# Performance work log

Hardware: AMD Instinct MI355X
Metric: run time of the kernel (lower is better)

The kernel has to match this reference:

```python
import jax, jax.numpy as jnp
import numpy as np

B, S, L, H, E, V = 32, 48, 48, 1024, 1024, 32000


def setup_inputs() -> dict:
    key = jax.random.key(0)
    ks = jax.random.split(key, 16)
    s = 0.02
    return {
        "label": jax.random.randint(ks[0], (B, S), 0, V),
        "init_hidden": jax.random.normal(ks[1], (1, B, H), jnp.float32),
        "encoder_output": jax.random.normal(ks[2], (B, L, H), jnp.float32),
        "emb": jax.random.normal(ks[3], (V, E), jnp.float32) * s,
        "attn_W": jax.random.normal(ks[4], (2 * H, L), jnp.float32) * s,
        "attn_b": jnp.zeros((L,), jnp.float32),
        "comb_W": jax.random.normal(ks[5], (2 * H, H), jnp.float32) * s,
        "comb_b": jnp.zeros((H,), jnp.float32),
        "W_ih": jax.random.normal(ks[6], (E, 3 * H), jnp.float32) * s,
        "W_hh": jax.random.normal(ks[7], (H, 3 * H), jnp.float32) * s,
        "b_ih": jnp.zeros((3 * H,), jnp.float32),
        "b_hh": jnp.zeros((3 * H,), jnp.float32),
        "out_W": jax.random.normal(ks[8], (H, V), jnp.float32) * s,
        "out_b": jnp.zeros((V,), jnp.float32),
    }


def _decode(label, init_hidden, encoder_output, emb, attn_W, attn_b,
            comb_W, comb_b, W_ih, W_hh, b_ih, b_hh, out_W, out_b):
    # Teacher forcing (teaching_force_rate=1.0): inputs are relu(embedding(label[:, i]))
    xs = jax.nn.relu(emb[label])            # (B, S, E)
    xs = jnp.transpose(xs, (1, 0, 2))       # (S, B, E) for scan

    def step(h, xe):                        # h: (B,H), xe: (B,E)
        # Attention: Linear(cat(emb, hidden)) -> nn.Softmax() on a 3D (B,1,L)
        # tensor, which in torch defaults to dim=0 (the batch dim) -- replicated.
        sim = jnp.concatenate([xe, h], axis=-1) @ attn_W + attn_b   # (B, L)
        w = jax.nn.softmax(sim, axis=0)                             # over batch (faithful)
        ctx = jnp.einsum('bl,blh->bh', w, encoder_output)           # bmm
        g = jax.nn.relu(jnp.concatenate([ctx, xe], axis=-1) @ comb_W + comb_b)  # (B,H)
        # Single GRU step (torch gate order: r, z, n)
        gx = g @ W_ih + b_ih
        gh = h @ W_hh + b_hh
        xr, xz, xn = jnp.split(gx, 3, axis=-1)
        hr, hz, hn = jnp.split(gh, 3, axis=-1)
        r = jax.nn.sigmoid(xr + hr)
        z = jax.nn.sigmoid(xz + hz)
        n = jnp.tanh(xn + r * hn)
        h_new = (1.0 - z) * n + z * h
        out = jax.nn.log_softmax(h_new @ out_W + out_b, axis=-1)    # (B, V)
        return h_new, out

    _, outs = jax.lax.scan(step, init_hidden[0], xs)   # outs: (S, B, V)
    return jnp.transpose(outs, (1, 0, 2))              # (B, S, V)


def reference(label, init_hidden, encoder_output, emb, attn_W, attn_b,
              comb_W, comb_b, W_ih, W_hh, b_ih, b_hh, out_W, out_b):
    return _decode(label, init_hidden, encoder_output, emb, attn_W, attn_b,
                   comb_W, comb_b, W_ih, W_hh, b_ih, b_hh, out_W, out_b)
```

## Files before the change

kernel.cpp:

```cpp
#include <hip/hip_runtime.h>

#define NB 32
#define NS 48
#define NL 48
#define NH 1024
#define NE 1024
#define NV 32000
#define NR (NS*NB)
#define K3H 3072
#define RA_BLOCKS 64
#define RB_BLOCKS 128
#define RC_BLOCKS 64
#define NBLK_FULL (RA_BLOCKS + RB_BLOCKS + RC_BLOCKS)

typedef unsigned short u16;
typedef __bf16 bf16x8 __attribute__((ext_vector_type(8)));
typedef unsigned short ushort8 __attribute__((ext_vector_type(8)));
typedef float f32x4 __attribute__((ext_vector_type(4)));
typedef unsigned int uint4v __attribute__((ext_vector_type(4)));

__device__ __forceinline__ float bf2f(u16 x) {
    union { unsigned u; float f; } c; c.u = ((unsigned)x) << 16; return c.f;
}
__device__ __forceinline__ u16 f2bf(float f) {
    union { float f; unsigned u; } c; c.f = f;
    unsigned r = (c.u + 0x7FFFu + ((c.u >> 16) & 1u)) >> 16;
    return (u16)r;
}
__device__ __forceinline__ f32x4 mfma16(bf16x8 a, bf16x8 b, f32x4 c) {
    return __builtin_amdgcn_mfma_f32_16x16x32_bf16(a, b, c, 0, 0, 0);
}
__device__ __forceinline__ void gld_lds16(const void* g, void* l) {
    __builtin_amdgcn_global_load_lds((const __attribute__((address_space(1))) void*)g,
                                     (__attribute__((address_space(3))) void*)l, 16, 0, 0);
}

__device__ __forceinline__ void st16_coh(void* p, uint4v v) {
    asm volatile("global_store_dwordx4 %0, %1, off sc0 sc1" :: "v"(p), "v"(v) : "memory");
}
__device__ __forceinline__ void waitb(const int* line, int tgt) {
    if (tgt <= 0) return;
    int guard = 0; int v;
    for (;;) {
        asm volatile("global_load_dword %0, %1, off sc0 sc1\n\ts_waitcnt vmcnt(0)"
                     : "=v"(v) : "v"(line) : "memory");
        if (v >= tgt) return;
        __builtin_amdgcn_s_sleep(1);
        if (++guard > (1 << 20)) return;
    }
}
__device__ __forceinline__ void arrive2(int* cnt, int* superc, int* bcast, int lineMask, int val) {
    asm volatile("s_waitcnt vmcnt(0)" ::: "memory");
    int prev = __hip_atomic_fetch_add(cnt, 1, __ATOMIC_RELAXED, __HIP_MEMORY_SCOPE_AGENT);
    if ((prev & lineMask) == lineMask) {
        int p2 = __hip_atomic_fetch_add(superc, 1, __ATOMIC_RELAXED, __HIP_MEMORY_SCOPE_AGENT);
        if ((p2 & 7) == 7) {
#pragma unroll
            for (int i = 0; i < 24; ++i)
                asm volatile("global_store_dword %0, %1, off sc0 sc1"
                             :: "v"(bcast + i * 64), "v"(val) : "memory");
        }
    }
}

__global__ __launch_bounds__(256) void transpose_cast(const float* __restrict__ src, int K, int N,
                                                      char* __restrict__ dst, int bf16out) {
    __shared__ float tile[32][33];
    int k0 = blockIdx.y * 32, n0 = blockIdx.x * 32;
    int tx = threadIdx.x & 31, ty = threadIdx.x >> 5;
    for (int i = 0; i < 4; ++i) {
        int n = n0 + tx;
        float v = (n < N) ? src[(size_t)(k0 + ty + i*8) * N + n] : 0.f;
        tile[ty + i*8][tx] = v;
    }
    __syncthreads();
    for (int i = 0; i < 4; ++i) {
        int n = n0 + ty + i*8;
        int k = k0 + tx;
        if (n < N) {
            float v = tile[tx][ty + i*8];
            if (bf16out) ((u16*)dst)[(size_t)n * K + k] = f2bf(v);
            else         ((float*)dst)[(size_t)n * K + k] = v;
        }
    }
}

__global__ __launch_bounds__(256) void prep_inputs(const int* __restrict__ label, const float* __restrict__ emb,
                                                   const float* __restrict__ enc, const float* __restrict__ inith,
                                                   u16* __restrict__ xe, u16* __restrict__ encb, u16* __restrict__ hallx) {
    int blk = blockIdx.x, t = threadIdx.x;
    if (blk < NR) {
        int s = blk >> 5, b = blk & 31;
        int lab = label[b * NS + s];
        const float* src = emb + (size_t)lab * NE;
        u16* dst = xe + (size_t)blk * NE;
        for (int i = t; i < NE; i += 256) { float v = src[i]; dst[i] = f2bf(v > 0.f ? v : 0.f); }
    } else if (blk < 2 * NR) {
        int r = blk - NR;
        const float* src = enc + (size_t)r * NH;
        u16* dst = encb + (size_t)r * NH;
        for (int i = t; i < NH; i += 256) dst[i] = f2bf(src[i]);
    } else {
        int b = blk - 2 * NR;
        const float* src = inith + (size_t)b * NH;
        u16* dst = hallx + (size_t)b * NH;
        for (int i = t; i < NH; i += 256) dst[i] = f2bf(src[i]);
    }
}

__global__ __launch_bounds__(384) void simxe2_kernel(const u16* __restrict__ xe, const u16* __restrict__ aw1t,
                                                     const float* __restrict__ attnB, float* __restrict__ simxe) {
    int r = blockIdx.x, t = threadIdx.x;
    int l = t >> 3, part = t & 7;
    const u16* x = xe + (size_t)r * 1024 + part * 128;
    const u16* ww = aw1t + (size_t)l * 1024 + part * 128;
    float acc = 0.f;
#pragma unroll
    for (int k = 0; k < 128; k += 8) {
        ushort8 xv = *reinterpret_cast<const ushort8*>(x + k);
        ushort8 wv = *reinterpret_cast<const ushort8*>(ww + k);
#pragma unroll
        for (int u = 0; u < 8; ++u) acc += bf2f(xv[u]) * bf2f(wv[u]);
    }
    acc += __shfl_xor(acc, 1);
    acc += __shfl_xor(acc, 2);
    acc += __shfl_xor(acc, 4);
    if (part == 0) simxe[(size_t)r * NL + l] = acc + attnB[l];
}

template<int MODE>
__global__ __launch_bounds__(256) void gemm_bf16(const u16* __restrict__ A, const u16* __restrict__ Bt,
                                                 void* __restrict__ Cout, const float* __restrict__ bias, int N) {
    __shared__ u16 ldsA[128 * 64];
    __shared__ u16 ldsB[128 * 64];
    const int t = threadIdx.x;
    const int lane = t & 63, w = t >> 6;
    const int wm = w >> 1, wn = w & 1;
    const int m0 = blockIdx.x * 128, n0 = blockIdx.y * 128;
    f32x4 acc[4][4] = {};
    for (int kt = 0; kt < 16; ++kt) {
        const int k0 = kt * 64;
#pragma unroll
        for (int i = 0; i < 4; ++i) {
            int chunk = i * 256 + t;
            int row = chunk >> 3, slot = chunk & 7;
            int srck = ((slot ^ (row & 7)) * 8);
            const u16* ga = A  + (size_t)(m0 + row) * 1024 + k0 + srck;
            const u16* gb = Bt + (size_t)(n0 + row) * 1024 + k0 + srck;
            u16* la = ldsA + (size_t)(i * 256 + w * 64) * 8;
            u16* lb = ldsB + (size_t)(i * 256 + w * 64) * 8;
            gld_lds16(ga, la);
            gld_lds16(gb, lb);
        }
        asm volatile("s_waitcnt vmcnt(0)" ::: "memory");
        __syncthreads();
#pragma unroll
        for (int kk = 0; kk < 2; ++kk) {
            bf16x8 a[4], b[4];
#pragma unroll
            for (int f = 0; f < 4; ++f) {
                int rowA = wm * 64 + f * 16 + (lane & 15);
                int slotA = (kk * 4 + (lane >> 4)) ^ (rowA & 7);
                a[f] = *reinterpret_cast<const bf16x8*>(ldsA + rowA * 64 + slotA * 8);
                int rowB = wn * 64 + f * 16 + (lane & 15);
                int slotB = (kk * 4 + (lane >> 4)) ^ (rowB & 7);
                b[f] = *reinterpret_cast<const bf16x8*>(ldsB + rowB * 64 + slotB * 8);
            }
#pragma unroll
            for (int fm = 0; fm < 4; ++fm)
#pragma unroll
                for (int fn = 0; fn < 4; ++fn)
                    acc[fm][fn] = mfma16(a[fm], b[fn], acc[fm][fn]);
        }
        __syncthreads();
    }
#pragma unroll
    for (int fm = 0; fm < 4; ++fm) {
#pragma unroll
        for (int fn = 0; fn < 4; ++fn) {
#pragma unroll
            for (int rr = 0; rr < 4; ++rr) {
                int m = m0 + wm * 64 + fm * 16 + (lane >> 4) * 4 + rr;
                int n = n0 + wn * 64 + fn * 16 + (lane & 15);
                float v = acc[fm][fn][rr];
                if (bias) v += bias[n];
                if (MODE == 0)      ((float*)Cout)[(size_t)m * N + n] = v;
                else if (MODE == 2) ((u16*)Cout)[(size_t)m * N + n] = f2bf(v);
                else if (MODE == 1)
                    ((float*)Cout)[((size_t)(m & 31) * NS + (m >> 5)) * NV + n] = v;
                else
                    ((u16*)Cout)[((size_t)(m & 31) * NS + (m >> 5)) * NV + n] = f2bf(v);
            }
        }
    }
}

__global__ __launch_bounds__(512) void recurrence8(
    const float* __restrict__ simxe, const u16* __restrict__ gxe,
    const u16* __restrict__ P, const u16* __restrict__ aw2t,
    const u16* __restrict__ whht, const u16* __restrict__ wiht,
    const float* __restrict__ b_ih, const float* __restrict__ b_hh,
    u16* __restrict__ g_rot, u16* __restrict__ hallx,
    const float* __restrict__ outW, const float* __restrict__ outB,
    u16* __restrict__ outWT, u16* __restrict__ logit, int* __restrict__ bar)
{
    __shared__ __align__(16) char smem[155776];
    int* cntA   = bar;
    int* cntB   = bar + 512;
    int* superA = bar + 1024;
    int* superB = bar + 1088;
    int* bcastA = bar + 1152;
    int* bcastB = bar + 2688;
    int* cntC   = bar + 4224;
    const int blk = blockIdx.x, t = threadIdx.x;
    const int lane = t & 63, w = t >> 6;
    const int r16 = lane & 15, kg = lane >> 4;

    if (blk < RA_BLOCKS) {
        int* myB = bcastB + (blk % 24) * 64;
        const int b = blk >> 1, half = blk & 1;
        u16*   W2T  = (u16*)smem;
        u16*   Pl   = (u16*)(smem + 99072);
        float* siml = (float*)(smem + 148224);
        float* wl   = (float*)(smem + 154496);
        u16*   gtmp = (u16*)(smem + 154752);
        for (int idx = t; idx < 48 * 1024; idx += 512) {
            int l = idx >> 10, k = idx & 1023;
            W2T[l * 1032 + k] = aw2t[idx];
        }
        for (int idx = t; idx < 48 * 512; idx += 512) {
            int l = idx >> 9, j = idx & 511;
            Pl[idx] = P[((size_t)(b * 48 + l)) * NH + half * 512 + j];
        }
        __syncthreads();
        const int mt = w & 1, nt = w >> 1;
        const int m0 = mt * 16, n0 = nt * 16;

        for (int s = 0; s < NS; ++s) {
            float gxev = bf2f(gxe[((size_t)(s * 32 + b)) * NH + half * 512 + t]);
            float sxv0 = 0.f, sxv1 = 0.f, sxv2 = 0.f, sxv3 = 0.f;
            if (w < 6) {
                const float* sxe = simxe + (size_t)(s * 32) * NL;
                sxv0 = sxe[(m0 + kg * 4 + 0) * NL + n0 + r16];
                sxv1 = sxe[(m0 + kg * 4 + 1) * NL + n0 + r16];
                sxv2 = sxe[(m0 + kg * 4 + 2) * NL + n0 + r16];
                sxv3 = sxe[(m0 + kg * 4 + 3) * NL + n0 + r16];
            }
            if (t == 0) waitb(myB, s);
            __syncthreads();
            const u16* hprev = hallx + (size_t)s * (NB * NH);
            if (w < 6) {
                f32x4 acc0; f32x4 acc1 = {};
                acc0[0] = sxv0; acc0[1] = sxv1; acc0[2] = sxv2; acc0[3] = sxv3;
                const u16* aP = hprev + (size_t)(m0 + r16) * NH + kg * 8;
                const u16* bP = W2T + (n0 + r16) * 1032 + kg * 8;
#pragma unroll
                for (int k = 0; k < 1024; k += 64) {
                    acc0 = mfma16(*reinterpret_cast<const bf16x8*>(aP + k),
                                  *reinterpret_cast<const bf16x8*>(bP + k), acc0);
                    acc1 = mfma16(*reinterpret_cast<const bf16x8*>(aP + k + 32),
                                  *reinterpret_cast<const bf16x8*>(bP + k + 32), acc1);
                }
#pragma unroll
                for (int rr = 0; rr < 4; ++rr)
                    siml[(m0 + kg * 4 + rr) * 49 + n0 + r16] = acc0[rr] + acc1[rr];
            }
            __syncthreads();
            if (t < 384) {
                int l = t >> 3, p = t & 7;
                float v0 = siml[(p * 4 + 0) * 49 + l];
                float v1 = siml[(p * 4 + 1) * 49 + l];
                float v2 = siml[(p * 4 + 2) * 49 + l];
                float v3 = siml[(p * 4 + 3) * 49 + l];
                float m = fmaxf(fmaxf(v0, v1), fmaxf(v2, v3));
                m = fmaxf(m, __shfl_xor(m, 1));
                m = fmaxf(m, __shfl_xor(m, 2));
                m = fmaxf(m, __shfl_xor(m, 4));
                float den = __expf(v0 - m) + __expf(v1 - m) + __expf(v2 - m) + __expf(v3 - m);
                den += __shfl_xor(den, 1);
                den += __shfl_xor(den, 2);
                den += __shfl_xor(den, 4);
                if (p == (b >> 2)) {
                    int bi = b & 3;
                    float vb = bi == 0 ? v0 : bi == 1 ? v1 : bi == 2 ? v2 : v3;
                    wl[l] = __expf(vb - m) / den;
                }
            }
            __syncthreads();
            {
                float acc = gxev;
#pragma unroll
                for (int l = 0; l < 48; ++l) acc += wl[l] * bf2f(Pl[l * 512 + t]);
                gtmp[t] = f2bf(fmaxf(acc, 0.f));
            }
            __syncthreads();
            if (t < 64) {
                uint4v v = *reinterpret_cast<const uint4v*>(gtmp + t * 8);
                st16_coh(g_rot + (size_t)s * (NB * NH) + (size_t)b * NH + half * 512 + t * 8, v);
            }
            if (t == 0) arrive2(cntA + (blk & 7) * 64, superA, bcastA, 7, s + 1);
        }
    } else if (blk < RA_BLOCKS + RB_BLOCKS) {
        const int rb = blk - RA_BLOCKS;
        int* myB = bcastB + (rb % 24) * 64;
        int* myA = bcastA + (rb % 24) * 64;
        const int c0 = rb * 8;
        u16*   Whh = (u16*)smem;
        u16*   Wih = (u16*)(smem + 66048);
        float* ghs = (float*)(smem + 132096);
        float* gxs = (float*)(smem + 140288);
        u16*   htmp = (u16*)(smem + 148480);
        for (int idx = t; idx < 32 * 1024; idx += 512) {
            int pr = idx >> 10, k = idx & 1023;
            u16 vh = 0, vi = 0;
            if (pr < 24) {
                size_t srow = (size_t)((pr >> 3) * 1024 + c0 + (pr & 7));
                vh = whht[srow * NH + k];
                vi = wiht[srow * NH + k];
            }
            Whh[pr * 1032 + k] = vh;
            Wih[pr * 1032 + k] = vi;
        }
        const int gb2 = (t & 255) >> 3, gcol = t & 7;
        const float bxr = b_ih[c0 + gcol], bxz = b_ih[1024 + c0 + gcol], bxn = b_ih[2048 + c0 + gcol];
        const float bhr = b_hh[c0 + gcol], bhz = b_hh[1024 + c0 + gcol], bhn = b_hh[2048 + c0 + gcol];
        __syncthreads();
        const int mt = (w >> 1) & 1, nt = w & 1, kh = w >> 2;
        const int m0 = mt * 16;

        for (int s = 0; s < NS; ++s) {
            if (t == 0) waitb(myB, s);
            __syncthreads();
            const u16* hprev = hallx + (size_t)s * (NB * NH);
            const u16* gcur  = g_rot + (size_t)s * (NB * NH);
            float hold = bf2f(hprev[(size_t)gb2 * NH + c0 + gcol]);
            {
                f32x4 acc0 = {}, acc1 = {};
                const u16* aP = hprev + (size_t)(m0 + r16) * NH + kh * 512 + kg * 8;
                const u16* bP = Whh + (nt * 16 + r16) * 1032 + kh * 512 + kg * 8;
#pragma unroll
                for (int k = 0; k < 512; k += 64) {
                    acc0 = mfma16(*reinterpret_cast<const bf16x8*>(aP + k),
                                  *reinterpret_cast<const bf16x8*>(bP + k), acc0);
                    acc1 = mfma16(*reinterpret_cast<const bf16x8*>(aP + k + 32),
                                  *reinterpret_cast<const bf16x8*>(bP + k + 32), acc1);
                }
#pragma unroll
                for (int rr = 0; rr < 4; ++rr)
                    ghs[kh * 1024 + (m0 + kg * 4 + rr) * 32 + nt * 16 + r16] = acc0[rr] + acc1[rr];
            }
            if (t == 0) waitb(myA, s + 1);
            __syncthreads();
            {
                f32x4 acc0 = {}, acc1 = {};
                const u16* aP = gcur + (size_t)(m0 + r16) * NH + kh * 512 + kg * 8;
                const u16* bP = Wih + (nt * 16 + r16) * 1032 + kh * 512 + kg * 8;
#pragma unroll
                for (int k = 0; k < 512; k += 64) {
                    acc0 = mfma16(*reinterpret_cast<const bf16x8*>(aP + k),
                                  *reinterpret_cast<const bf16x8*>(bP + k), acc0);
                    acc1 = mfma16(*reinterpret_cast<const bf16x8*>(aP + k + 32),
                                  *reinterpret_cast<const bf16x8*>(bP + k + 32), acc1);
                }
#pragma unroll
                for (int rr = 0; rr < 4; ++rr)
                    gxs[kh * 1024 + (m0 + kg * 4 + rr) * 32 + nt * 16 + r16] = acc0[rr] + acc1[rr];
            }
            __syncthreads();
            if (t < 256) {
                float gxr = gxs[gb2 * 32 + gcol]      + gxs[1024 + gb2 * 32 + gcol]      + bxr;
                float gxz = gxs[gb2 * 32 + 8 + gcol]  + gxs[1024 + gb2 * 32 + 8 + gcol]  + bxz;
                float gxn = gxs[gb2 * 32 + 16 + gcol] + gxs[1024 + gb2 * 32 + 16 + gcol] + bxn;
                float ghr = ghs[gb2 * 32 + gcol]      + ghs[1024 + gb2 * 32 + gcol]      + bhr;
                float ghz = ghs[gb2 * 32 + 8 + gcol]  + ghs[1024 + gb2 * 32 + 8 + gcol]  + bhz;
                float ghn = ghs[gb2 * 32 + 16 + gcol] + ghs[1024 + gb2 * 32 + 16 + gcol] + bhn;
                float rg = 1.f / (1.f + __expf(-(gxr + ghr)));
                float zg = 1.f / (1.f + __expf(-(gxz + ghz)));
                float ng = tanhf(gxn + rg * ghn);
                float hnew = (1.f - zg) * ng + zg * hold;
                htmp[t] = f2bf(hnew);
            }
            __syncthreads();
            if (t < 32) {
                uint4v v = *reinterpret_cast<const uint4v*>(htmp + t * 8);
                st16_coh(hallx + ((size_t)(s + 1) * NB + t) * NH + c0, v);
            }
            if (t == 0) arrive2(cntB + (rb & 7) * 64, superB, bcastB, 15, s + 1);
        }
    } else {
        const int rc = blk - (RA_BLOCKS + RB_BLOCKS);
        {
            float* ttile = (float*)smem;
            const int sub = t >> 7, u = t & 127;
            for (int T0 = 0; T0 < 32000; T0 += 256) {
                int T = T0 + rc * 4 + sub;
                int tn = T >> 5, tk = T & 31;
                int n0 = tn * 32, k0 = tk * 32;
                __syncthreads();
#pragma unroll
                for (int j = 0; j < 8; ++j) {
                    int e = j * 128 + u;
                    int row = e >> 5, col = e & 31;
                    ttile[(sub * 32 + row) * 33 + col] = outW[(size_t)(k0 + row) * NV + n0 + col];
                }
                __syncthreads();
                int nr = u >> 2, kc = u & 3;
                unsigned pk0, pk1, pk2, pk3;
                {
                    const float* base = ttile + (sub * 32 + kc * 8) * 33 + nr;
                    pk0 = (unsigned)f2bf(base[0])      | ((unsigned)f2bf(base[33])  << 16);
                    pk1 = (unsigned)f2bf(base[66])     | ((unsigned)f2bf(base[99])  << 16);
                    pk2 = (unsigned)f2bf(base[132])    | ((unsigned)f2bf(base[165]) << 16);
                    pk3 = (unsigned)f2bf(base[198])    | ((unsigned)f2bf(base[231]) << 16);
                }
                uint4v v; v[0] = pk0; v[1] = pk1; v[2] = pk2; v[3] = pk3;
                st16_coh(outWT + (size_t)(n0 + nr) * NH + k0 + kc * 8, v);
            }
            asm volatile("s_waitcnt vmcnt(0)" ::: "memory");
            __syncthreads();
            if (t == 0) {
                __hip_atomic_fetch_add(cntC, 1, __ATOMIC_RELAXED, __HIP_MEMORY_SCOPE_AGENT);
                waitb(cntC, RC_BLOCKS);
            }
            __syncthreads();
        }
        u16* ldsA = (u16*)smem;
        u16* ldsB = (u16*)(smem + 16384);
        const u16* Ab = hallx + NB * NH;
        const int wm = w >> 2, wn = w & 3;
        int lastReady = 0;
        for (int T = rc; T < 3000; T += RC_BLOCKS) {
            int mt = T / 250, nt = T - mt * 250;
            int need = 4 * mt + 4;
            if (need > lastReady) {
                if (t == 0) waitb(bcastB + (rc % 24) * 64, need);
                lastReady = need;
            }
            __syncthreads();
            const int m0 = mt * 128, n0 = nt * 128;
            f32x4 acc[4][2] = {};
            for (int kt = 0; kt < 16; ++kt) {
                const int k0 = kt * 64;
#pragma unroll
                for (int i = 0; i < 2; ++i) {
                    int chunk = i * 512 + t;
                    int row = chunk >> 3, slot = chunk & 7;
                    int srck = ((slot ^ (row & 7)) * 8);
                    gld_lds16(Ab    + (size_t)(m0 + row) * 1024 + k0 + srck,
                              ldsA + (size_t)(i * 512 + w * 64) * 8);
                    gld_lds16(outWT + (size_t)(n0 + row) * 1024 + k0 + srck,
                              ldsB + (size_t)(i * 512 + w * 64) * 8);
                }
                asm volatile("s_waitcnt vmcnt(0)" ::: "memory");
                __syncthreads();
#pragma unroll
                for (int kk = 0; kk < 2; ++kk) {
                    bf16x8 a[4], bb[2];
#pragma unroll
                    for (int f = 0; f < 4; ++f) {
                        int rowA = wm * 64 + f * 16 + r16;
                        int slotA = (kk * 4 + kg) ^ (rowA & 7);
                        a[f] = *reinterpret_cast<const bf16x8*>(ldsA + rowA * 64 + slotA * 8);
                    }
#pragma unroll
                    for (int f = 0; f < 2; ++f) {
                        int rowB = wn * 32 + f * 16 + r16;
                        int slotB = (kk * 4 + kg) ^ (rowB & 7);
                        bb[f] = *reinterpret_cast<const bf16x8*>(ldsB + rowB * 64 + slotB * 8);
                    }
#pragma unroll
                    for (int fm = 0; fm < 4; ++fm)
#pragma unroll
                        for (int fn = 0; fn < 2; ++fn)
                            acc[fm][fn] = mfma16(a[fm], bb[fn], acc[fm][fn]);
                }
                __syncthreads();
            }
#pragma unroll
            for (int fm = 0; fm < 4; ++fm) {
#pragma unroll
                for (int fn = 0; fn < 2; ++fn) {
#pragma unroll
                    for (int rr = 0; rr < 4; ++rr) {
                        int m = m0 + wm * 64 + fm * 16 + kg * 4 + rr;
                        int n = n0 + wn * 32 + fn * 16 + r16;
                        float v = acc[fm][fn][rr] + outB[n];
                        logit[((size_t)(m & 31) * NS + (m >> 5)) * NV + n] = f2bf(v);
                    }
                }
            }
        }
    }
}

__global__ __launch_bounds__(256) void logsoftmax_kernel(float* __restrict__ out) {
    __shared__ float red[8];
    float* row = out + (size_t)blockIdx.x * NV;
    int t = threadIdx.x;
    float m = -1e30f;
    for (int i = t; i < NV; i += 256) m = fmaxf(m, row[i]);
    for (int o = 32; o >= 1; o >>= 1) m = fmaxf(m, __shfl_xor(m, o));
    if ((t & 63) == 0) red[t >> 6] = m;
    __syncthreads();
    m = fmaxf(fmaxf(red[0], red[1]), fmaxf(red[2], red[3]));
    float sum = 0.f;
    for (int i = t; i < NV; i += 256) sum += __expf(row[i] - m);
    for (int o = 32; o >= 1; o >>= 1) sum += __shfl_xor(sum, o);
    if ((t & 63) == 0) red[4 + (t >> 6)] = sum;
    __syncthreads();
    sum = (red[4] + red[5]) + (red[6] + red[7]);
    float lse = m + __logf(sum);
    for (int i = t; i < NV; i += 256) row[i] = row[i] - lse;
}

__global__ __launch_bounds__(512) void logsoftmax_bf16(const u16* __restrict__ lg, float* __restrict__ out) {
    __shared__ __align__(16) u16 rowb[NV];
    __shared__ float red[16];
    const u16* src = lg + (size_t)blockIdx.x * NV;
    float* dst = out + (size_t)blockIdx.x * NV;
    int t = threadIdx.x;
    for (int i = t; i < NV / 8; i += 512)
        ((ushort8*)rowb)[i] = ((const ushort8*)src)[i];
    __syncthreads();
    float m = -1e30f;
    for (int i = t; i < NV; i += 512) m = fmaxf(m, bf2f(rowb[i]));
    for (int o = 32; o >= 1; o >>= 1) m = fmaxf(m, __shfl_xor(m, o));
    if ((t & 63) == 0) red[t >> 6] = m;
    __syncthreads();
    m = red[0];
#pragma unroll
    for (int i = 1; i < 8; ++i) m = fmaxf(m, red[i]);
    float sum = 0.f;
    for (int i = t; i < NV; i += 512) sum += __expf(bf2f(rowb[i]) - m);
    for (int o = 32; o >= 1; o >>= 1) sum += __shfl_xor(sum, o);
    if ((t & 63) == 0) red[8 + (t >> 6)] = sum;
    __syncthreads();
    sum = 0.f;
#pragma unroll
    for (int i = 0; i < 8; ++i) sum += red[8 + i];
    float lse = m + __logf(sum);
    for (int i = t; i < NV; i += 512) dst[i] = bf2f(rowb[i]) - lse;
}

extern "C" void kernel_launch(void* const* d_in, const int* in_sizes, int n_in,
                              void* d_out, int out_size, void* d_ws, size_t ws_size,
                              hipStream_t stream) {
    const int*   label = (const int*)  d_in[0];
    const float* inith = (const float*)d_in[1];
    const float* enc   = (const float*)d_in[2];
    const float* emb   = (const float*)d_in[3];
    const float* attnW = (const float*)d_in[4];
    const float* attnB = (const float*)d_in[5];
    const float* combW = (const float*)d_in[6];
    const float* combB = (const float*)d_in[7];
    const float* Wih   = (const float*)d_in[8];
    const float* Whh   = (const float*)d_in[9];
    const float* bih   = (const float*)d_in[10];
    const float* bhh   = (const float*)d_in[11];
    const float* outW  = (const float*)d_in[12];
    const float* outB  = (const float*)d_in[13];
    char* ws = (char*)d_ws;

    size_t BAR_OFF    = 0;
    size_t OUTWT_OFF  = 32768;
    size_t WHHT_OFF   = OUTWT_OFF + (size_t)NV*NH*2;
    size_t WIHT_OFF   = WHHT_OFF + (size_t)K3H*NH*2;
    size_t CW1T_OFF   = WIHT_OFF + (size_t)K3H*NH*2;
    size_t CW2T_OFF   = CW1T_OFF + (size_t)NH*NH*2;
    size_t AW2T_OFF   = CW2T_OFF + (size_t)NH*NH*2;
    size_t AW1T_OFF   = AW2T_OFF + (size_t)NL*NH*2;
    size_t XE_OFF     = AW2T_OFF + (size_t)NL*NH*4;
    size_t ENCB_OFF   = XE_OFF   + (size_t)NR*NE*2;
    size_t SIMXE_OFF  = ENCB_OFF + (size_t)NR*NH*2;
    size_t GXE_OFF    = SIMXE_OFF+ (size_t)NR*NL*4;
    size_t P_OFF      = GXE_OFF  + (size_t)NR*NH*2;
    size_t HALL_OFF   = P_OFF    + (size_t)NR*NH*2;
    size_t GROT_OFF   = HALL_OFF + (size_t)(NS+1)*NB*NH*2;
    size_t LOGIT_OFF  = GROT_OFF + (size_t)NS*NB*NH*2;
    size_t TOTAL_NEED = LOGIT_OFF+ (size_t)NR*NV*2;

    int*   bar   = (int*)(ws + BAR_OFF);
    u16*   outWT = (u16*)(ws + OUTWT_OFF);
    u16*   whht  = (u16*)(ws + WHHT_OFF);
    u16*   wiht  = (u16*)(ws + WIHT_OFF);
    u16*   cw1t  = (u16*)(ws + CW1T_OFF);
    u16*   cw2t  = (u16*)(ws + CW2T_OFF);
    u16*   aw2t  = (u16*)(ws + AW2T_OFF);
    u16*   aw1t  = (u16*)(ws + AW1T_OFF);
    u16*   xe    = (u16*)(ws + XE_OFF);
    u16*   encb  = (u16*)(ws + ENCB_OFF);
    float* simxe = (float*)(ws + SIMXE_OFF);
    u16*   gxe   = (u16*)(ws + GXE_OFF);
    u16*   Pb    = (u16*)(ws + P_OFF);
    u16*   hallx = (u16*)(ws + HALL_OFF);
    u16*   grot  = (u16*)(ws + GROT_OFF);
    u16*   logit = (u16*)(ws + LOGIT_OFF);

    hipMemsetAsync(bar, 0, 32768, stream);
    prep_inputs<<<2 * NR + NB, 256, 0, stream>>>(label, emb, enc, inith, xe, encb, hallx);

    transpose_cast<<<dim3(K3H / 32, 32), 256, 0, stream>>>(Whh, NH, K3H, (char*)whht, 1);
    transpose_cast<<<dim3(K3H / 32, 32), 256, 0, stream>>>(Wih, NH, K3H, (char*)wiht, 1);
    transpose_cast<<<dim3(NH / 32, 32), 256, 0, stream>>>(combW, NH, NH, (char*)cw1t, 1);
    transpose_cast<<<dim3(NH / 32, 32), 256, 0, stream>>>(combW + (size_t)NH * NH, NH, NH, (char*)cw2t, 1);
    transpose_cast<<<dim3(2, 32), 256, 0, stream>>>(attnW + (size_t)NH * NL, NH, NL, (char*)aw2t, 1);
    transpose_cast<<<dim3(2, 32), 256, 0, stream>>>(attnW, NH, NL, (char*)aw1t, 1);

    simxe2_kernel<<<NR, 384, 0, stream>>>(xe, aw1t, attnB, simxe);
    gemm_bf16<2><<<dim3(NR / 128, NH / 128), 256, 0, stream>>>(xe, cw2t, gxe, combB, NH);
    gemm_bf16<2><<<dim3(NR / 128, NH / 128), 256, 0, stream>>>(encb, cw1t, Pb, nullptr, NH);

    if (ws_size >= TOTAL_NEED) {
        recurrence8<<<NBLK_FULL, 512, 0, stream>>>(simxe, gxe, Pb, aw2t, whht, wiht,
                                                   bih, bhh, grot, hallx,
                                                   outW, outB, outWT, logit, bar);
        logsoftmax_bf16<<<NR, 512, 0, stream>>>(logit, (float*)d_out);
    } else {
        transpose_cast<<<dim3(NV / 32, 32), 256, 0, stream>>>(outW, NH, NV, (char*)outWT, 1);
        recurrence8<<<RA_BLOCKS + RB_BLOCKS, 512, 0, stream>>>(simxe, gxe, Pb, aw2t, whht, wiht,
                                                               bih, bhh, grot, hallx,
                                                               outW, outB, outWT, logit, bar);
        gemm_bf16<1><<<dim3(NR / 128, NV / 128), 256, 0, stream>>>(hallx + (size_t)NB * NH, outWT, d_out, outB, NV);
        logsoftmax_kernel<<<NR, 256, 0, stream>>>((float*)d_out);
    }
}
```

Baseline: 1.038 ms.

## Use 256-row output tiles and let recurrence blocks drain final GEMM tiles

The output-projection GEMM inside the persistent recurrence kernel now uses 256x128 tiles, covering eight timesteps per row tile instead of four. The dedicated GEMM blocks process the first five row tiles as the hidden states become ready. After the recurrence finishes, all blocks (attention, GRU and GEMM) pull the last row tile's 250 column tiles from a shared atomic work queue. The aim is to spread the tail GEMM work, which otherwise runs only on 64 blocks, across all 256 blocks. The log-softmax kernel also moves from 512 to 1024 threads per row. Risks include coarser readiness granularity that delays when GEMM work can start, and heavier register pressure from the larger tiles.

```diff
diff --git a/kernel.cpp b/kernel.cpp
--- a/kernel.cpp
+++ b/kernel.cpp
@@ -195,14 +195,92 @@
     }
 }
 
-__global__ __launch_bounds__(512) void recurrence8(
+__device__ __forceinline__ void do_tile256(char* smem, const u16* Ab, const u16* outWT,
+                                           const float* outB, u16* logit,
+                                           int mt, int nt, int t) {
+    u16* ldsA = (u16*)smem;
+    u16* ldsB = (u16*)(smem + 32768);
+    const int w = t >> 6, lane = t & 63;
+    const int r16 = lane & 15, kg = lane >> 4;
+    const int wm = w >> 1, wn = w & 1;
+    const int m0 = mt * 256, n0 = nt * 128;
+    f32x4 acc[4][4] = {};
+    for (int kt = 0; kt < 16; ++kt) {
+        const int k0 = kt * 64;
+#pragma unroll
+        for (int i = 0; i < 4; ++i) {
+            int chunk = i * 512 + t;
+            int row = chunk >> 3, slot = chunk & 7;
+            int srck = ((slot ^ (row & 7)) * 8);
+            gld_lds16(Ab + (size_t)(m0 + row) * 1024 + k0 + srck,
+                      ldsA + (size_t)(i * 512 + w * 64) * 8);
+        }
+#pragma unroll
+        for (int i = 0; i < 2; ++i) {
+            int chunk = i * 512 + t;
+            int row = chunk >> 3, slot = chunk & 7;
+            int srck = ((slot ^ (row & 7)) * 8);
+            gld_lds16(outWT + (size_t)(n0 + row) * 1024 + k0 + srck,
+                      ldsB + (size_t)(i * 512 + w * 64) * 8);
+        }
+        asm volatile("s_waitcnt vmcnt(0)" ::: "memory");
+        __syncthreads();
+#pragma unroll
+        for (int kk = 0; kk < 2; ++kk) {
+            bf16x8 a[4], b[4];
+#pragma unroll
+            for (int f = 0; f < 4; ++f) {
+                int rowA = wm * 64 + f * 16 + r16;
+                int slotA = (kk * 4 + kg) ^ (rowA & 7);
+                a[f] = *reinterpret_cast<const bf16x8*>(ldsA + rowA * 64 + slotA * 8);
+                int rowB = wn * 64 + f * 16 + r16;
+                int slotB = (kk * 4 + kg) ^ (rowB & 7);
+                b[f] = *reinterpret_cast<const bf16x8*>(ldsB + rowB * 64 + slotB * 8);
+            }
+#pragma unroll
+            for (int fm = 0; fm < 4; ++fm)
+#pragma unroll
+                for (int fn = 0; fn < 4; ++fn)
+                    acc[fm][fn] = mfma16(a[fm], b[fn], acc[fm][fn]);
+        }
+        __syncthreads();
+    }
+#pragma unroll
+    for (int fm = 0; fm < 4; ++fm) {
+#pragma unroll
+        for (int fn = 0; fn < 4; ++fn) {
+#pragma unroll
+            for (int rr = 0; rr < 4; ++rr) {
+                int m = m0 + wm * 64 + fm * 16 + kg * 4 + rr;
+                int n = n0 + wn * 64 + fn * 16 + r16;
+                float v = acc[fm][fn][rr] + outB[n];
+                logit[((size_t)(m & 31) * NS + (m >> 5)) * NV + n] = f2bf(v);
+            }
+        }
+    }
+}
+
+__device__ __forceinline__ void queue_gemm(char* smem, int* qslot, int* qcnt,
+                                           const u16* Ab, const u16* outWT,
+                                           const float* outB, u16* logit, int t) {
+    for (;;) {
+        __syncthreads();
+        if (t == 0) *qslot = __hip_atomic_fetch_add(qcnt, 1, __ATOMIC_RELAXED, __HIP_MEMORY_SCOPE_AGENT);
+        __syncthreads();
+        int nt = *qslot;
+        if (nt >= 250) return;
+        do_tile256(smem, Ab, outWT, outB, logit, 5, nt, t);
+    }
+}
+
+__global__ __launch_bounds__(512) void recurrence9(
     const float* __restrict__ simxe, const u16* __restrict__ gxe,
     const u16* __restrict__ P, const u16* __restrict__ aw2t,
     const u16* __restrict__ whht, const u16* __restrict__ wiht,
     const float* __restrict__ b_ih, const float* __restrict__ b_hh,
     u16* __restrict__ g_rot, u16* __restrict__ hallx,
     const float* __restrict__ outW, const float* __restrict__ outB,
-    u16* __restrict__ outWT, u16* __restrict__ logit, int* __restrict__ bar)
+    u16* __restrict__ outWT, u16* __restrict__ logit, int* __restrict__ bar, int fused)
 {
     __shared__ __align__(16) char smem[155776];
     int* cntA   = bar;
@@ -212,9 +290,12 @@
     int* bcastA = bar + 1152;
     int* bcastB = bar + 2688;
     int* cntC   = bar + 4224;
+    int* qcnt   = bar + 4288;
+    int* qslot  = (int*)(smem + 153600);
     const int blk = blockIdx.x, t = threadIdx.x;
     const int lane = t & 63, w = t >> 6;
     const int r16 = lane & 15, kg = lane >> 4;
+    const u16* Ab = hallx + NB * NH;
 
     if (blk < RA_BLOCKS) {
         int* myB = bcastB + (blk % 24) * 64;
@@ -300,6 +381,11 @@
             }
             if (t == 0) arrive2(cntA + (blk & 7) * 64, superA, bcastA, 7, s + 1);
         }
+        if (fused) {
+            if (t == 0) { waitb(myB, 48); waitb(cntC, RC_BLOCKS); }
+            __syncthreads();
+            queue_gemm(smem, qslot, qcnt, Ab, outWT, outB, logit, t);
+        }
     } else if (blk < RA_BLOCKS + RB_BLOCKS) {
         const int rb = blk - RA_BLOCKS;
         int* myB = bcastB + (rb % 24) * 64;
@@ -387,6 +473,11 @@
             }
             if (t == 0) arrive2(cntB + (rb & 7) * 64, superB, bcastB, 15, s + 1);
         }
+        if (fused) {
+            if (t == 0) { waitb(myB, 48); waitb(cntC, RC_BLOCKS); }
+            __syncthreads();
+            queue_gemm(smem, qslot, qcnt, Ab, outWT, outB, logit, t);
+        }
     } else {
         const int rc = blk - (RA_BLOCKS + RB_BLOCKS);
         {
@@ -408,10 +499,10 @@
                 unsigned pk0, pk1, pk2, pk3;
                 {
                     const float* base = ttile + (sub * 32 + kc * 8) * 33 + nr;
-                    pk0 = (unsigned)f2bf(base[0])      | ((unsigned)f2bf(base[33])  << 16);
-                    pk1 = (unsigned)f2bf(base[66])     | ((unsigned)f2bf(base[99])  << 16);
-                    pk2 = (unsigned)f2bf(base[132])    | ((unsigned)f2bf(base[165]) << 16);
-                    pk3 = (unsigned)f2bf(base[198])    | ((unsigned)f2bf(base[231]) << 16);
+                    pk0 = (unsigned)f2bf(base[0])   | ((unsigned)f2bf(base[33])  << 16);
+                    pk1 = (unsigned)f2bf(base[66])  | ((unsigned)f2bf(base[99])  << 16);
+                    pk2 = (unsigned)f2bf(base[132]) | ((unsigned)f2bf(base[165]) << 16);
+                    pk3 = (unsigned)f2bf(base[198]) | ((unsigned)f2bf(base[231]) << 16);
                 }
                 uint4v v; v[0] = pk0; v[1] = pk1; v[2] = pk2; v[3] = pk3;
                 st16_coh(outWT + (size_t)(n0 + nr) * NH + k0 + kc * 8, v);
@@ -424,72 +515,20 @@
             }
             __syncthreads();
         }
-        u16* ldsA = (u16*)smem;
-        u16* ldsB = (u16*)(smem + 16384);
-        const u16* Ab = hallx + NB * NH;
-        const int wm = w >> 2, wn = w & 3;
         int lastReady = 0;
-        for (int T = rc; T < 3000; T += RC_BLOCKS) {
+        for (int T = rc; T < 1250; T += RC_BLOCKS) {
             int mt = T / 250, nt = T - mt * 250;
-            int need = 4 * mt + 4;
+            int need = 8 * mt + 8;
             if (need > lastReady) {
                 if (t == 0) waitb(bcastB + (rc % 24) * 64, need);
                 lastReady = need;
             }
             __syncthreads();
-            const int m0 = mt * 128, n0 = nt * 128;
-            f32x4 acc[4][2] = {};
-            for (int kt = 0; kt < 16; ++kt) {
-                const int k0 = kt * 64;
-#pragma unroll
-                for (int i = 0; i < 2; ++i) {
-                    int chunk = i * 512 + t;
-                    int row = chunk >> 3, slot = chunk & 7;
-                    int srck = ((slot ^ (row & 7)) * 8);
-                    gld_lds16(Ab    + (size_t)(m0 + row) * 1024 + k0 + srck,
-                              ldsA + (size_t)(i * 512 + w * 64) * 8);
-                    gld_lds16(outWT + (size_t)(n0 + row) * 1024 + k0 + srck,
-                              ldsB + (size_t)(i * 512 + w * 64) * 8);
-                }
-                asm volatile("s_waitcnt vmcnt(0)" ::: "memory");
-                __syncthreads();
-#pragma unroll
-                for (int kk = 0; kk < 2; ++kk) {
-                    bf16x8 a[4], bb[2];
-#pragma unroll
-                    for (int f = 0; f < 4; ++f) {
-                        int rowA = wm * 64 + f * 16 + r16;
-                        int slotA = (kk * 4 + kg) ^ (rowA & 7);
-                        a[f] = *reinterpret_cast<const bf16x8*>(ldsA + rowA * 64 + slotA * 8);
-                    }
-#pragma unroll
-                    for (int f = 0; f < 2; ++f) {
-                        int rowB = wn * 32 + f * 16 + r16;
-                        int slotB = (kk * 4 + kg) ^ (rowB & 7);
-                        bb[f] = *reinterpret_cast<const bf16x8*>(ldsB + rowB * 64 + slotB * 8);
-                    }
-#pragma unroll
-                    for (int fm = 0; fm < 4; ++fm)
-#pragma unroll
-                        for (int fn = 0; fn < 2; ++fn)
-                            acc[fm][fn] = mfma16(a[fm], bb[fn], acc[fm][fn]);
-                }
-                __syncthreads();
-            }
-#pragma unroll
-            for (int fm = 0; fm < 4; ++fm) {
-#pragma unroll
-                for (int fn = 0; fn < 2; ++fn) {
-#pragma unroll
-                    for (int rr = 0; rr < 4; ++rr) {
-                        int m = m0 + wm * 64 + fm * 16 + kg * 4 + rr;
-                        int n = n0 + wn * 32 + fn * 16 + r16;
-                        float v = acc[fm][fn][rr] + outB[n];
-                        logit[((size_t)(m & 31) * NS + (m >> 5)) * NV + n] = f2bf(v);
-                    }
-                }
-            }
-        }
+            do_tile256(smem, Ab, outWT, outB, logit, mt, nt, t);
+        }
+        if (t == 0) waitb(bcastB + (rc % 24) * 64, 48);
+        __syncthreads();
+        queue_gemm(smem, qslot, qcnt, Ab, outWT, outB, logit, t);
     }
 }
 
@@ -513,33 +552,33 @@
     for (int i = t; i < NV; i += 256) row[i] = row[i] - lse;
 }
 
-__global__ __launch_bounds__(512) void logsoftmax_bf16(const u16* __restrict__ lg, float* __restrict__ out) {
+__global__ __launch_bounds__(1024) void logsoftmax_bf16(const u16* __restrict__ lg, float* __restrict__ out) {
     __shared__ __align__(16) u16 rowb[NV];
-    __shared__ float red[16];
+    __shared__ float red[32];
     const u16* src = lg + (size_t)blockIdx.x * NV;
     float* dst = out + (size_t)blockIdx.x * NV;
     int t = threadIdx.x;
-    for (int i = t; i < NV / 8; i += 512)
+    for (int i = t; i < NV / 8; i += 1024)
         ((ushort8*)rowb)[i] = ((const ushort8*)src)[i];
     __syncthreads();
     float m = -1e30f;
-    for (int i = t; i < NV; i += 512) m = fmaxf(m, bf2f(rowb[i]));
+    for (int i = t; i < NV; i += 1024) m = fmaxf(m, bf2f(rowb[i]));
     for (int o = 32; o >= 1; o >>= 1) m = fmaxf(m, __shfl_xor(m, o));
     if ((t & 63) == 0) red[t >> 6] = m;
     __syncthreads();
     m = red[0];
 #pragma unroll
-    for (int i = 1; i < 8; ++i) m = fmaxf(m, red[i]);
+    for (int i = 1; i < 16; ++i) m = fmaxf(m, red[i]);
     float sum = 0.f;
-    for (int i = t; i < NV; i += 512) sum += __expf(bf2f(rowb[i]) - m);
+    for (int i = t; i < NV; i += 1024) sum += __expf(bf2f(rowb[i]) - m);
     for (int o = 32; o >= 1; o >>= 1) sum += __shfl_xor(sum, o);
-    if ((t & 63) == 0) red[8 + (t >> 6)] = sum;
+    if ((t & 63) == 0) red[16 + (t >> 6)] = sum;
     __syncthreads();
     sum = 0.f;
 #pragma unroll
-    for (int i = 0; i < 8; ++i) sum += red[8 + i];
+    for (int i = 0; i < 16; ++i) sum += red[16 + i];
     float lse = m + __logf(sum);
-    for (int i = t; i < NV; i += 512) dst[i] = bf2f(rowb[i]) - lse;
+    for (int i = t; i < NV; i += 1024) dst[i] = bf2f(rowb[i]) - lse;
 }
 
 extern "C" void kernel_launch(void* const* d_in, const int* in_sizes, int n_in,
@@ -611,15 +650,15 @@
     gemm_bf16<2><<<dim3(NR / 128, NH / 128), 256, 0, stream>>>(encb, cw1t, Pb, nullptr, NH);
 
     if (ws_size >= TOTAL_NEED) {
-        recurrence8<<<NBLK_FULL, 512, 0, stream>>>(simxe, gxe, Pb, aw2t, whht, wiht,
+        recurrence9<<<NBLK_FULL, 512, 0, stream>>>(simxe, gxe, Pb, aw2t, whht, wiht,
                                                    bih, bhh, grot, hallx,
-                                                   outW, outB, outWT, logit, bar);
-        logsoftmax_bf16<<<NR, 512, 0, stream>>>(logit, (float*)d_out);
+                                                   outW, outB, outWT, logit, bar, 1);
+        logsoftmax_bf16<<<NR, 1024, 0, stream>>>(logit, (float*)d_out);
     } else {
         transpose_cast<<<dim3(NV / 32, 32), 256, 0, stream>>>(outW, NH, NV, (char*)outWT, 1);
-        recurrence8<<<RA_BLOCKS + RB_BLOCKS, 512, 0, stream>>>(simxe, gxe, Pb, aw2t, whht, wiht,
+        recurrence9<<<RA_BLOCKS + RB_BLOCKS, 512, 0, stream>>>(simxe, gxe, Pb, aw2t, whht, wiht,
                                                                bih, bhh, grot, hallx,
-                                                               outW, outB, outWT, logit, bar);
+                                                               outW, outB, outWT, logit, bar, 0);
         gemm_bf16<1><<<dim3(NR / 128, NV / 128), 256, 0, stream>>>(hallx + (size_t)NB * NH, outWT, d_out, outB, NV);
         logsoftmax_kernel<<<NR, 256, 0, stream>>>((float*)d_out);
     }
```

Measured after the change: 922.9 us. -11.1%, faster.
